# Kernel optimization log

Hardware: AMD Instinct MI355X
Metric: run time of the kernel (lower is better)

## Reference

```python
import jax, jax.numpy as jnp
import numpy as np

NEG_INF = -1.0e15  # matches the module's self.infty


def setup_inputs() -> dict:
    key = jax.random.key(0)
    ks = jax.random.split(key, 12)
    B, N, D, H, HD = 256, 1024, 128, 8, 16
    inp = {
        "x": jax.random.normal(ks[0], (B, N, D), dtype=jnp.float32),
        "h_g": jax.random.normal(ks[1], (B, D), dtype=jnp.float32),
        "first": jax.random.normal(ks[2], (B, D), dtype=jnp.float32),
        "last": jax.random.normal(ks[3], (B, D), dtype=jnp.float32),
        "context": jax.random.normal(ks[4], (B, 2), dtype=jnp.float32),
        "K": jax.random.normal(ks[5], (B, H, N, HD), dtype=jnp.float32),
        "V": jax.random.normal(ks[6], (B, H, N, HD), dtype=jnp.float32),
        "K_lg": jax.random.normal(ks[7], (B, N, D), dtype=jnp.float32),
        "Wq": jax.random.normal(ks[8], (D, 3 * D + 2), dtype=jnp.float32) * 0.05,
        "bq": jnp.zeros((D,), dtype=jnp.float32),
        "Wo": jax.random.normal(ks[9], (D, D), dtype=jnp.float32) * 0.05,
        "bo": jnp.zeros((D,), dtype=jnp.float32),
        "mask": jax.random.randint(ks[10], (B, N), 0, 2, dtype=jnp.int32),
        "t": 1,
    }
    return inp


def reference(x, h_g, first, last, context, K, V, K_lg, Wq, bq, Wo, bo, mask, t):
    B, N, D = x.shape
    H, HD = K.shape[1], K.shape[3]
    # t > 0 path: context vector from graph embedding + first/last visited nodes
    h_c = jnp.concatenate([h_g, first, last, context], axis=1)  # [B, 3D+2]
    Q = h_c @ Wq.T + bq                                          # [B, D]
    Q = Q.reshape(B, H, HD)                                      # single query per head
    # masked single-query multi-head attention
    scale = jnp.sqrt(jnp.asarray(HD, dtype=x.dtype))
    scores = jnp.einsum("bhd,bhnd->bhn", Q, K) / scale          # [B, H, N]
    scores = jnp.where(mask[:, None, :] == 0, NEG_INF, scores)
    attn = jax.nn.softmax(scores, axis=-1)
    u = jnp.einsum("bhn,bhnd->bhd", attn, V).reshape(B, D)       # [B, D]
    u = u @ Wo.T + bo
    # pointer logits with tanh clipping
    logits = jnp.einsum("bd,bnd->bn", u, K_lg) / jnp.sqrt(jnp.asarray(D, dtype=x.dtype))
    logits = 10.0 * jnp.tanh(logits)
    logits = jnp.where(mask == 0, NEG_INF, logits)
    p = jax.nn.softmax(logits, axis=1)                           # [B, N]
    vertexes = jnp.argmax(p, axis=1)[:, None]                    # greedy (sample=False)
    probs = jnp.take_along_axis(p, vertexes, axis=1)             # [B, 1]
    return vertexes, probs
```

## Files before the change

kernel.cpp:

```cpp
#include <hip/hip_runtime.h>
#include <math.h>

#define Bn 256
#define Nn 1024
#define Dn 128
#define Hn 8
#define HDn 16
#define NEG_INF -1.0e15f

__global__ __launch_bounds__(128) void k_q(
    const float* __restrict__ h_g, const float* __restrict__ first,
    const float* __restrict__ last, const float* __restrict__ context,
    const float* __restrict__ Wq, const float* __restrict__ bq,
    float* __restrict__ Qout)
{
    __shared__ __align__(16) float hc[3 * Dn + 2];
    const int b = blockIdx.x;
    const int t = threadIdx.x;
    hc[t]          = h_g[b * Dn + t];
    hc[Dn + t]     = first[b * Dn + t];
    hc[2 * Dn + t] = last[b * Dn + t];
    if (t < 2) hc[3 * Dn + t] = context[b * 2 + t];
    __syncthreads();

    const float2* w2 = (const float2*)(Wq + (size_t)t * (3 * Dn + 2));
    const float2* h2 = (const float2*)hc;
    float acc = bq[t];
#pragma unroll 8
    for (int k = 0; k < (3 * Dn + 2) / 2; ++k) {
        float2 w = w2[k], h = h2[k];
        acc = fmaf(w.x, h.x, fmaf(w.y, h.y, acc));
    }
    Qout[b * Dn + t] = acc;
}

__global__ __launch_bounds__(512, 4) void k_attn(
    const float* __restrict__ Q, const float* __restrict__ K,
    const float* __restrict__ V, const int* __restrict__ mask,
    float* __restrict__ Uout)
{
    __shared__ float sQ[64];
    __shared__ float sPart[512][17];
    __shared__ float sOut[64];
    __shared__ float sSum[4];

    const int blk = blockIdx.x;
    const int b = blk >> 1, pr = blk & 1;
    const int tid = threadIdx.x;
    const int hl = tid >> 7;
    const int h = pr * 4 + hl;
    const int lh = tid & 127;

    if (tid < 64) sQ[tid] = Q[b * Dn + pr * 64 + tid];

    const int* __restrict__ mrow = mask + (size_t)b * Nn;
    int mk[8];
#pragma unroll
    for (int i = 0; i < 8; ++i) mk[i] = mrow[lh + 128 * i];

    __syncthreads();
    float4 q4[4];
#pragma unroll
    for (int j = 0; j < 4; ++j) q4[j] = ((const float4*)(sQ + hl * 16))[j];

    const float4* __restrict__ Kp = (const float4*)(K + ((size_t)b * Hn + h) * Nn * HDn);
    const float4* __restrict__ Vp = (const float4*)(V + ((size_t)b * Hn + h) * Nn * HDn);

    float4 kb[2][4], vb[2][4];
#pragma unroll
    for (int j = 0; j < 4; ++j) {
        kb[0][j] = Kp[(size_t)lh * 4 + j];
        vb[0][j] = Vp[(size_t)lh * 4 + j];
    }

    float4 u0 = {0,0,0,0}, u1 = {0,0,0,0}, u2 = {0,0,0,0}, u3 = {0,0,0,0};
    float sum = 0.f;

#pragma unroll
    for (int i = 0; i < 8; ++i) {
        const int cur = i & 1, nxt = cur ^ 1;
        if (i < 7) {
            const int n = lh + 128 * (i + 1);
#pragma unroll
            for (int j = 0; j < 4; ++j) {
                kb[nxt][j] = Kp[(size_t)n * 4 + j];
                vb[nxt][j] = Vp[(size_t)n * 4 + j];
            }
        }
        __builtin_amdgcn_sched_barrier(0);
        float s = 0.f;
#pragma unroll
        for (int j = 0; j < 4; ++j) {
            s = fmaf(q4[j].x, kb[cur][j].x, s);
            s = fmaf(q4[j].y, kb[cur][j].y, s);
            s = fmaf(q4[j].z, kb[cur][j].z, s);
            s = fmaf(q4[j].w, kb[cur][j].w, s);
        }
        const float e = mk[i] ? __expf(s * 0.25f) : 0.f;
        sum += e;
        u0.x = fmaf(e, vb[cur][0].x, u0.x); u0.y = fmaf(e, vb[cur][0].y, u0.y);
        u0.z = fmaf(e, vb[cur][0].z, u0.z); u0.w = fmaf(e, vb[cur][0].w, u0.w);
        u1.x = fmaf(e, vb[cur][1].x, u1.x); u1.y = fmaf(e, vb[cur][1].y, u1.y);
        u1.z = fmaf(e, vb[cur][1].z, u1.z); u1.w = fmaf(e, vb[cur][1].w, u1.w);
        u2.x = fmaf(e, vb[cur][2].x, u2.x); u2.y = fmaf(e, vb[cur][2].y, u2.y);
        u2.z = fmaf(e, vb[cur][2].z, u2.z); u2.w = fmaf(e, vb[cur][2].w, u2.w);
        u3.x = fmaf(e, vb[cur][3].x, u3.x); u3.y = fmaf(e, vb[cur][3].y, u3.y);
        u3.z = fmaf(e, vb[cur][3].z, u3.z); u3.w = fmaf(e, vb[cur][3].w, u3.w);
    }

    {
        float* p = sPart[tid];
        p[0]=u0.x; p[1]=u0.y; p[2]=u0.z; p[3]=u0.w;
        p[4]=u1.x; p[5]=u1.y; p[6]=u1.z; p[7]=u1.w;
        p[8]=u2.x; p[9]=u2.y; p[10]=u2.z; p[11]=u2.w;
        p[12]=u3.x; p[13]=u3.y; p[14]=u3.z; p[15]=u3.w;
        p[16]=sum;
    }
    __syncthreads();

    if (tid < 64) {
        const int hh = tid >> 4, d = tid & 15;
        float a = 0.f;
#pragma unroll 8
        for (int j = 0; j < 128; ++j) a += sPart[hh * 128 + j][d];
        sOut[tid] = a;
    } else if (tid < 68) {
        const int hh = tid - 64;
        float a = 0.f;
#pragma unroll 8
        for (int j = 0; j < 128; ++j) a += sPart[hh * 128 + j][16];
        sSum[hh] = a;
    }
    __syncthreads();
    if (tid < 64) {
        Uout[b * Dn + pr * 64 + tid] = sOut[tid] / sSum[tid >> 4];
    }
}

__global__ __launch_bounds__(1024) void k_ptr(
    const float* __restrict__ U, const float* __restrict__ Wo,
    const float* __restrict__ bo, const float* __restrict__ K_lg,
    const int* __restrict__ mask, float* __restrict__ out)
{
    __shared__ __align__(16) float sU[Dn];
    __shared__ __align__(16) float sU2[Dn];
    __shared__ __align__(16) float sL[Nn];
    __shared__ float sRv[16];
    __shared__ int   sRi[16];
    __shared__ float sRs[16];

    const int b = blockIdx.x;
    const int tid = threadIdx.x;
    const int lane = tid & 63, wave = tid >> 6;

    if (tid < Dn) sU[tid] = U[b * Dn + tid];
    __syncthreads();
    {
        const int d = tid >> 3, e8 = tid & 7;
        const float4* wrow = (const float4*)(Wo + (size_t)d * Dn + e8 * 16);
        const float4* su4 = (const float4*)(sU + e8 * 16);
        float acc = 0.f;
#pragma unroll
        for (int k = 0; k < 4; ++k) {
            const float4 w = wrow[k], u = su4[k];
            acc = fmaf(w.x, u.x, fmaf(w.y, u.y, fmaf(w.z, u.z, fmaf(w.w, u.w, acc))));
        }
        acc += __shfl_xor(acc, 1, 64);
        acc += __shfl_xor(acc, 2, 64);
        acc += __shfl_xor(acc, 4, 64);
        if (e8 == 0) sU2[d] = acc + bo[d];
    }
    __syncthreads();

    const float4* __restrict__ Kl = (const float4*)(K_lg + (size_t)b * Nn * Dn);
    const int* __restrict__ mrow = mask + (size_t)b * Nn;
    const int grp = tid >> 5, l32 = tid & 31;
    const float4 u2f = ((const float4*)sU2)[l32];
    const float sc = 0.08838834764831845f;
#pragma unroll
    for (int it0 = 0; it0 < 32; it0 += 4) {
        float4 kl[4];
#pragma unroll
        for (int j = 0; j < 4; ++j)
            kl[j] = Kl[(size_t)(grp + 32 * (it0 + j)) * 32 + l32];
        __builtin_amdgcn_sched_barrier(0);
#pragma unroll
        for (int j = 0; j < 4; ++j) {
            float p = kl[j].x * u2f.x + kl[j].y * u2f.y + kl[j].z * u2f.z + kl[j].w * u2f.w;
#pragma unroll
            for (int o = 16; o >= 1; o >>= 1) p += __shfl_xor(p, o, 64);
            if (l32 == 0) {
                const int n = grp + 32 * (it0 + j);
                sL[n] = (mrow[n] == 0) ? NEG_INF : 10.0f * tanhf(p * sc);
            }
        }
    }
    __syncthreads();

    float bv = sL[tid]; int bi = tid;
#pragma unroll
    for (int o = 32; o >= 1; o >>= 1) {
        const float ov = __shfl_xor(bv, o, 64);
        const int oi = __shfl_xor(bi, o, 64);
        if (ov > bv || (ov == bv && oi < bi)) { bv = ov; bi = oi; }
    }
    if (lane == 0) { sRv[wave] = bv; sRi[wave] = bi; }
    __syncthreads();
    bv = sRv[0]; bi = sRi[0];
#pragma unroll
    for (int w = 1; w < 16; ++w) {
        const float ov = sRv[w]; const int oi = sRi[w];
        if (ov > bv || (ov == bv && oi < bi)) { bv = ov; bi = oi; }
    }

    float lsum = __expf(sL[tid] - bv);
#pragma unroll
    for (int o = 32; o >= 1; o >>= 1) lsum += __shfl_xor(lsum, o, 64);
    if (lane == 0) sRs[wave] = lsum;
    __syncthreads();
    if (tid == 0) {
        float tot = 0.f;
#pragma unroll
        for (int w = 0; w < 16; ++w) tot += sRs[w];
        out[b] = (float)bi;
        out[Bn + b] = 1.0f / tot;
    }
}

extern "C" void kernel_launch(void* const* d_in, const int* in_sizes, int n_in,
                              void* d_out, int out_size, void* d_ws, size_t ws_size,
                              hipStream_t stream) {
    const float* h_g     = (const float*)d_in[1];
    const float* first   = (const float*)d_in[2];
    const float* last    = (const float*)d_in[3];
    const float* context = (const float*)d_in[4];
    const float* K       = (const float*)d_in[5];
    const float* V       = (const float*)d_in[6];
    const float* K_lg    = (const float*)d_in[7];
    const float* Wq      = (const float*)d_in[8];
    const float* bq      = (const float*)d_in[9];
    const float* Wo      = (const float*)d_in[10];
    const float* bo      = (const float*)d_in[11];
    const int*   mask    = (const int*)d_in[12];
    float* out = (float*)d_out;

    float* Qws = (float*)d_ws;
    float* Uws = Qws + Bn * Dn;

    k_q   <<<Bn,      128, 0, stream>>>(h_g, first, last, context, Wq, bq, Qws);
    k_attn<<<Bn * 2,  512, 0, stream>>>(Qws, K, V, mask, Uws);
    k_ptr <<<Bn,     1024, 0, stream>>>(Uws, Wo, bo, K_lg, mask, out);
}
```

Baseline: 117.4 us.

## Stream K/V through LDS with async global_load_lds triple buffering in attention

Rewrites the attention kernel so each block handles one (batch, head) pair with 128 threads. K and V chunks are loaded straight into LDS with global_load_lds and triple buffered, using vmcnt waits and barriers. A rotated read order reduces LDS bank conflicts. The goal is deeper memory-level parallelism and overlap of loads with compute on a bandwidth-bound kernel, in exchange for more LDS per block and more raw barriers, plus hand-written waitcnt logic that is fragile if the compiler reorders code.

```diff
diff --git a/kernel.cpp b/kernel.cpp
--- a/kernel.cpp
+++ b/kernel.cpp
@@ -7,6 +7,15 @@
 #define Hn 8
 #define HDn 16
 #define NEG_INF -1.0e15f
+
+#define AS(n) __attribute__((address_space(n)))
+#define WAITV(n) asm volatile("s_waitcnt vmcnt(" #n ")" ::: "memory")
+
+__device__ __forceinline__ void gl_lds16(const float* g, float* l) {
+    __builtin_amdgcn_global_load_lds(
+        (AS(1) void*)(unsigned long long)g,
+        (AS(3) void*)l, 16, 0, 0);
+}
 
 __global__ __launch_bounds__(128) void k_q(
     const float* __restrict__ h_g, const float* __restrict__ first,
@@ -34,106 +43,113 @@
     Qout[b * Dn + t] = acc;
 }
 
-__global__ __launch_bounds__(512, 4) void k_attn(
+__global__ __launch_bounds__(128) void k_attn(
     const float* __restrict__ Q, const float* __restrict__ K,
     const float* __restrict__ V, const int* __restrict__ mask,
     float* __restrict__ Uout)
 {
-    __shared__ float sQ[64];
-    __shared__ float sPart[512][17];
-    __shared__ float sOut[64];
-    __shared__ float sSum[4];
-
-    const int blk = blockIdx.x;
-    const int b = blk >> 1, pr = blk & 1;
+    __shared__ __align__(16) float sK[3 * 2048];
+    __shared__ __align__(16) float sV[3 * 2048];
+    __shared__ float sTot;
+
+    const int bh = blockIdx.x;
+    const int b = bh >> 3, h = bh & 7;
     const int tid = threadIdx.x;
-    const int hl = tid >> 7;
-    const int h = pr * 4 + hl;
-    const int lh = tid & 127;
-
-    if (tid < 64) sQ[tid] = Q[b * Dn + pr * 64 + tid];
 
     const int* __restrict__ mrow = mask + (size_t)b * Nn;
     int mk[8];
 #pragma unroll
-    for (int i = 0; i < 8; ++i) mk[i] = mrow[lh + 128 * i];
-
-    __syncthreads();
+    for (int c = 0; c < 8; ++c) mk[c] = mrow[c * 128 + tid];
     float4 q4[4];
 #pragma unroll
-    for (int j = 0; j < 4; ++j) q4[j] = ((const float4*)(sQ + hl * 16))[j];
-
-    const float4* __restrict__ Kp = (const float4*)(K + ((size_t)b * Hn + h) * Nn * HDn);
-    const float4* __restrict__ Vp = (const float4*)(V + ((size_t)b * Hn + h) * Nn * HDn);
-
-    float4 kb[2][4], vb[2][4];
-#pragma unroll
-    for (int j = 0; j < 4; ++j) {
-        kb[0][j] = Kp[(size_t)lh * 4 + j];
-        vb[0][j] = Vp[(size_t)lh * 4 + j];
-    }
-
+    for (int j = 0; j < 4; ++j)
+        q4[j] = ((const float4*)(Q + (size_t)b * Dn + h * HDn))[j];
+    WAITV(0);
+    __builtin_amdgcn_sched_barrier(0);
+
+    const float4* __restrict__ Kg = (const float4*)(K + (size_t)bh * Nn * HDn);
+    const float4* __restrict__ Vg = (const float4*)(V + (size_t)bh * Nn * HDn);
+
+#define STAGE(c, buf)                                                        \
+    {                                                                        \
+        const int g0 = (c) * 512 + tid;                                      \
+        _Pragma("unroll")                                                    \
+        for (int rr = 0; rr < 4; ++rr)                                       \
+            gl_lds16((const float*)(Kg + g0 + rr * 128),                     \
+                     sK + (buf) * 2048 + (rr * 128 + tid) * 4);              \
+        _Pragma("unroll")                                                    \
+        for (int rr = 0; rr < 4; ++rr)                                       \
+            gl_lds16((const float*)(Vg + g0 + rr * 128),                     \
+                     sV + (buf) * 2048 + (rr * 128 + tid) * 4);              \
+    }
+
+    STAGE(0, 0);
+    STAGE(1, 1);
+
+    const int rot = (tid >> 1) & 3;
     float4 u0 = {0,0,0,0}, u1 = {0,0,0,0}, u2 = {0,0,0,0}, u3 = {0,0,0,0};
     float sum = 0.f;
 
 #pragma unroll
-    for (int i = 0; i < 8; ++i) {
-        const int cur = i & 1, nxt = cur ^ 1;
-        if (i < 7) {
-            const int n = lh + 128 * (i + 1);
-#pragma unroll
-            for (int j = 0; j < 4; ++j) {
-                kb[nxt][j] = Kp[(size_t)n * 4 + j];
-                vb[nxt][j] = Vp[(size_t)n * 4 + j];
-            }
-        }
+    for (int c = 0; c < 8; ++c) {
+        if (c < 7) { WAITV(8); } else { WAITV(0); }
         __builtin_amdgcn_sched_barrier(0);
+        __builtin_amdgcn_s_barrier();
+        __builtin_amdgcn_sched_barrier(0);
+        if (c < 6) {
+            if ((c & 1) == 0) { STAGE(c + 2, (c + 2) % 3); }
+            else              { STAGE(c + 2, (c + 2) % 3); }
+        }
+        const float4* kb4 = (const float4*)(sK + (c % 3) * 2048);
+        const float4* vb4 = (const float4*)(sV + (c % 3) * 2048);
         float s = 0.f;
+        float4 kgr[4];
 #pragma unroll
         for (int j = 0; j < 4; ++j) {
-            s = fmaf(q4[j].x, kb[cur][j].x, s);
-            s = fmaf(q4[j].y, kb[cur][j].y, s);
-            s = fmaf(q4[j].z, kb[cur][j].z, s);
-            s = fmaf(q4[j].w, kb[cur][j].w, s);
-        }
-        const float e = mk[i] ? __expf(s * 0.25f) : 0.f;
+            const int jj = (j + rot) & 3;
+            kgr[jj] = kb4[tid * 4 + jj];
+        }
+#pragma unroll
+        for (int jj = 0; jj < 4; ++jj) {
+            s = fmaf(q4[jj].x, kgr[jj].x, s);
+            s = fmaf(q4[jj].y, kgr[jj].y, s);
+            s = fmaf(q4[jj].z, kgr[jj].z, s);
+            s = fmaf(q4[jj].w, kgr[jj].w, s);
+        }
+        const float e = mk[c] ? __expf(s * 0.25f) : 0.f;
         sum += e;
-        u0.x = fmaf(e, vb[cur][0].x, u0.x); u0.y = fmaf(e, vb[cur][0].y, u0.y);
-        u0.z = fmaf(e, vb[cur][0].z, u0.z); u0.w = fmaf(e, vb[cur][0].w, u0.w);
-        u1.x = fmaf(e, vb[cur][1].x, u1.x); u1.y = fmaf(e, vb[cur][1].y, u1.y);
-        u1.z = fmaf(e, vb[cur][1].z, u1.z); u1.w = fmaf(e, vb[cur][1].w, u1.w);
-        u2.x = fmaf(e, vb[cur][2].x, u2.x); u2.y = fmaf(e, vb[cur][2].y, u2.y);
-        u2.z = fmaf(e, vb[cur][2].z, u2.z); u2.w = fmaf(e, vb[cur][2].w, u2.w);
-        u3.x = fmaf(e, vb[cur][3].x, u3.x); u3.y = fmaf(e, vb[cur][3].y, u3.y);
-        u3.z = fmaf(e, vb[cur][3].z, u3.z); u3.w = fmaf(e, vb[cur][3].w, u3.w);
-    }
-
+#pragma unroll
+        for (int j = 0; j < 4; ++j) {
+            const int jj = (j + rot) & 3;
+            const float4 vv = vb4[tid * 4 + jj];
+            if (jj == 0) { u0.x=fmaf(e,vv.x,u0.x); u0.y=fmaf(e,vv.y,u0.y); u0.z=fmaf(e,vv.z,u0.z); u0.w=fmaf(e,vv.w,u0.w); }
+            else if (jj == 1) { u1.x=fmaf(e,vv.x,u1.x); u1.y=fmaf(e,vv.y,u1.y); u1.z=fmaf(e,vv.z,u1.z); u1.w=fmaf(e,vv.w,u1.w); }
+            else if (jj == 2) { u2.x=fmaf(e,vv.x,u2.x); u2.y=fmaf(e,vv.y,u2.y); u2.z=fmaf(e,vv.z,u2.z); u2.w=fmaf(e,vv.w,u2.w); }
+            else { u3.x=fmaf(e,vv.x,u3.x); u3.y=fmaf(e,vv.y,u3.y); u3.z=fmaf(e,vv.z,u3.z); u3.w=fmaf(e,vv.w,u3.w); }
+        }
+    }
+#undef STAGE
+
+    __builtin_amdgcn_s_barrier();
+    float* P = sK;
     {
-        float* p = sPart[tid];
+        float* p = P + tid * 17;
         p[0]=u0.x; p[1]=u0.y; p[2]=u0.z; p[3]=u0.w;
         p[4]=u1.x; p[5]=u1.y; p[6]=u1.z; p[7]=u1.w;
         p[8]=u2.x; p[9]=u2.y; p[10]=u2.z; p[11]=u2.w;
         p[12]=u3.x; p[13]=u3.y; p[14]=u3.z; p[15]=u3.w;
         p[16]=sum;
     }
-    __syncthreads();
-
-    if (tid < 64) {
-        const int hh = tid >> 4, d = tid & 15;
-        float a = 0.f;
-#pragma unroll 8
-        for (int j = 0; j < 128; ++j) a += sPart[hh * 128 + j][d];
-        sOut[tid] = a;
-    } else if (tid < 68) {
-        const int hh = tid - 64;
-        float a = 0.f;
-#pragma unroll 8
-        for (int j = 0; j < 128; ++j) a += sPart[hh * 128 + j][16];
-        sSum[hh] = a;
-    }
-    __syncthreads();
-    if (tid < 64) {
-        Uout[b * Dn + pr * 64 + tid] = sOut[tid] / sSum[tid >> 4];
+    __builtin_amdgcn_s_barrier();
+    float acc = 0.f;
+    if (tid < 17) {
+#pragma unroll 16
+        for (int j = 0; j < 128; ++j) acc += P[j * 17 + tid];
+        if (tid == 16) sTot = acc;
+    }
+    __builtin_amdgcn_s_barrier();
+    if (tid < 16) {
+        Uout[(size_t)b * Dn + h * HDn + tid] = acc / sTot;
     }
 }
 
@@ -248,6 +264,6 @@
     float* Uws = Qws + Bn * Dn;
 
     k_q   <<<Bn,      128, 0, stream>>>(h_g, first, last, context, Wq, bq, Qws);
-    k_attn<<<Bn * 2,  512, 0, stream>>>(Qws, K, V, mask, Uws);
+    k_attn<<<Bn * Hn, 128, 0, stream>>>(Qws, K, V, mask, Uws);
     k_ptr <<<Bn,     1024, 0, stream>>>(Uws, Wo, bo, K_lg, mask, out);
 }
```

Result: slower. 152.1 us (+29.5%).
